# Performance work log

Measured on AMD Instinct MI355X. Metric: run time of the kernel, lower is better.

## Reference

```python
import jax, jax.numpy as jnp
import numpy as np

N, D, H, L, T, R = 50000, 128, 8, 2, 4, 8
E = 800000
HD = D // H  # head_size = 16
SQRT_D = float(np.sqrt(HD))


def typed_linear(x, types, W):
    # x: (n, Din), types: (n,), W: (T, Din, Dout)  -- per-type dense projection
    out = jnp.zeros((x.shape[0], W.shape[-1]), x.dtype)
    for t in range(W.shape[0]):
        out = out + jnp.where((types == t)[:, None], x @ W[t], 0.0)
    return out


def rel_typed(x, etype, W):
    # x: (E, H, d), etype: (E,), W: (H, R, d, d) -- per-head, per-edge-type linear
    out = jnp.zeros_like(x)
    for r in range(W.shape[1]):
        out = out + jnp.where((etype == r)[:, None, None], jnp.einsum('ehd,hdo->eho', x, W[:, r]), 0.0)
    return out


def edge_softmax(a, dst, n):
    # softmax over incoming edges per destination node, per head. a: (E, H)
    amax = jax.ops.segment_max(a, dst, num_segments=n)
    amax = jnp.where(jnp.isfinite(amax), amax, 0.0)
    ex = jnp.exp(a - amax[dst])
    s = jax.ops.segment_sum(ex, dst, num_segments=n)
    return ex / (s[dst] + 1e-9)


def layer_norm(x, g, b, eps=1e-5):
    mu = x.mean(-1, keepdims=True)
    var = ((x - mu) ** 2).mean(-1, keepdims=True)
    return (x - mu) * jax.lax.rsqrt(var + eps) * g + b


def hgt_conv(x, ntype, etype, src, dst, Wk, Wq, Wv, Wa, ratt, rmsg, rpri, skip):
    n = x.shape[0]
    k = typed_linear(x, ntype, Wk).reshape(n, H, HD)
    q = typed_linear(x, ntype, Wq).reshape(n, H, HD)
    v = typed_linear(x, ntype, Wv).reshape(n, H, HD)
    kw = rel_typed(k[src], etype, ratt)               # (E, H, d)
    pri = rpri[:, etype].T                            # (E, H)
    a = (kw * q[dst]).sum(-1) * pri / SQRT_D          # (E, H)
    m = rel_typed(v[src], etype, rmsg)                # (E, H, d)
    att = edge_softmax(a, dst, n)                     # (E, H)
    h = jax.ops.segment_sum(m * att[..., None], dst, num_segments=n)
    h = h.reshape(n, D)
    h = typed_linear(h, ntype, Wa)                    # dropout off (eval)
    alpha = jax.nn.sigmoid(skip[ntype])[:, None]
    return h * alpha + x * (1.0 - alpha)


def setup_inputs() -> dict:
    key = jax.random.key(0)
    ks = jax.random.split(key, 12)
    g_lin = float(np.sqrt(2.0 / (D + D)))   # xavier-ish scale for D x D
    g_rel = float(np.sqrt(2.0 / (HD + HD)))
    g_emb = float(np.sqrt(2.0 / (N + D)))
    return {
        'embed': jax.random.normal(ks[0], (T, N, D), jnp.float32) * g_emb,
        'Wk': jax.random.normal(ks[1], (L, T, D, D), jnp.float32) * g_lin,
        'Wq': jax.random.normal(ks[2], (L, T, D, D), jnp.float32) * g_lin,
        'Wv': jax.random.normal(ks[3], (L, T, D, D), jnp.float32) * g_lin,
        'Wa': jax.random.normal(ks[4], (L, T, D, D), jnp.float32) * g_lin,
        'rel_att': jax.random.normal(ks[5], (L, H, R, HD, HD), jnp.float32) * g_rel,
        'rel_msg': jax.random.normal(ks[6], (L, H, R, HD, HD), jnp.float32) * g_rel,
        'rel_pri': jnp.ones((L, H, R), jnp.float32),
        'skip': jnp.ones((L, T), jnp.float32),
        'ln_g': jnp.ones((L, D), jnp.float32),
        'ln_b': jnp.zeros((L, D), jnp.float32),
        'src': jax.random.randint(ks[7], (E,), 0, N, jnp.int32),
        'dst': jax.random.randint(ks[8], (E,), 0, N, jnp.int32),
        'ntype': jax.random.randint(ks[9], (N,), 0, T, jnp.int32),
        'etype': jax.random.randint(ks[10], (E,), 0, R, jnp.int32),
    }


def reference(embed, Wk, Wq, Wv, Wa, rel_att, rel_msg, rel_pri, skip, ln_g, ln_b, src, dst, ntype, etype):
    # masked per-type embedding init: node gets row <rank-within-its-type> of its type table
    onehot = jax.nn.one_hot(ntype, T, dtype=jnp.int32)
    rank = jnp.take_along_axis(jnp.cumsum(onehot, axis=0), ntype[:, None], axis=1)[:, 0] - 1
    h = embed[ntype, rank]                            # (N, D)
    for l in range(L):
        h_prev = h
        hc = hgt_conv(h, ntype, etype, src, dst,
                      Wk[l], Wq[l], Wv[l], Wa[l],
                      rel_att[l], rel_msg[l], rel_pri[l], skip[l])
        h = layer_norm(hc, ln_g[l], ln_b[l]) + h_prev
    return h
```

## Files before the change

### kernel.cpp

```cpp
#include <hip/hip_runtime.h>
#include <math.h>

#define N_NODES 50000
#define DIM     128
#define NHEAD   8
#define HDIM    16
#define NLAYER  2
#define NTYPE   4
#define NREL    8
#define NEDGE   800000
#define RB      256
#define MT      32
#define NK      (N_NODES * NREL)
#define LHR     (NLAYER * NHEAD * NREL)

typedef __attribute__((ext_vector_type(8))) short bf16x8;
typedef __attribute__((ext_vector_type(4))) float f32x4;

__device__ __forceinline__ float blo(unsigned w) { return __uint_as_float(w << 16); }
__device__ __forceinline__ float bhi(unsigned w) { return __uint_as_float(w & 0xFFFF0000u); }
__device__ __forceinline__ unsigned short f2bf(float f) {
    unsigned b = __float_as_uint(f);
    b += 0x7FFFu + ((b >> 16) & 1u);
    return (unsigned short)(b >> 16);
}
__device__ __forceinline__ bf16x8 pack8(float4 x0, float4 x1) {
    bf16x8 r;
    r[0] = (short)f2bf(x0.x); r[1] = (short)f2bf(x0.y);
    r[2] = (short)f2bf(x0.z); r[3] = (short)f2bf(x0.w);
    r[4] = (short)f2bf(x1.x); r[5] = (short)f2bf(x1.y);
    r[6] = (short)f2bf(x1.z); r[7] = (short)f2bf(x1.w);
    return r;
}
__device__ __forceinline__ bf16x8 zero8() {
    bf16x8 r;
    #pragma unroll
    for (int j = 0; j < 8; j++) r[j] = 0;
    return r;
}


__global__ void k_hist(const int* __restrict__ ntype, int* __restrict__ hist, int n) {
    __shared__ int cnt[NTYPE];
    if (threadIdx.x < NTYPE) cnt[threadIdx.x] = 0;
    __syncthreads();
    int i = blockIdx.x * RB + threadIdx.x;
    if (i < n) atomicAdd(&cnt[ntype[i]], 1);
    __syncthreads();
    if (threadIdx.x < NTYPE) hist[blockIdx.x * NTYPE + threadIdx.x] = cnt[threadIdx.x];
}

__global__ void k_prefix(const int* __restrict__ hist, int* __restrict__ off, int nb) {
    int t = threadIdx.x;
    if (t >= NTYPE) return;
    int acc = 0;
    for (int b = 0; b < nb; b++) { off[b * NTYPE + t] = acc; acc += hist[b * NTYPE + t]; }
}

__global__ void k_rank(const int* __restrict__ ntype, const int* __restrict__ off,
                       int* __restrict__ rank, int n) {
    __shared__ int ty[RB];
    int i = blockIdx.x * RB + threadIdx.x;
    int t = (i < n) ? ntype[i] : -1;
    ty[threadIdx.x] = t;
    __syncthreads();
    if (i < n) {
        int c = 0;
        for (int j = 0; j < (int)threadIdx.x; j++) c += (ty[j] == t);
        rank[i] = off[blockIdx.x * NTYPE + t] + c;
    }
}

__global__ void k_embed(const float* __restrict__ embed, const int* __restrict__ ntype,
                        const int* __restrict__ rank, float* __restrict__ h) {
    int i = blockIdx.x;
    int t = ntype[i], r = rank[i];
    h[(size_t)i * DIM + threadIdx.x] = embed[((size_t)t * N_NODES + r) * DIM + threadIdx.x];
}

__global__ void k_typeoff(const int* __restrict__ hist, const int* __restrict__ boff,
                          int nb, int* __restrict__ typeoff) {
    if (threadIdx.x == 0 && blockIdx.x == 0) {
        int acc = 0;
        for (int t = 0; t < NTYPE; t++) {
            typeoff[t] = acc;
            acc += boff[(nb - 1) * NTYPE + t] + hist[(nb - 1) * NTYPE + t];
        }
    }
}

__global__ void k_perm(const int* __restrict__ ntype, const int* __restrict__ rank,
                       const int* __restrict__ typeoff, int* __restrict__ perm,
                       int* __restrict__ iperm, int n) {
    int i = blockIdx.x * 256 + threadIdx.x;
    if (i < n) {
        int p = typeoff[ntype[i]] + rank[i];
        perm[p] = i;
        iperm[i] = p;
    }
}


__global__ void k_deg2(const int* __restrict__ dst, const int* __restrict__ etype,
                       int* __restrict__ deg) {
    int e = blockIdx.x * 256 + threadIdx.x;
    if (e < NEDGE) atomicAdd(&deg[dst[e] * NREL + etype[e]], 1);
}

__global__ void k_scan1(const int* __restrict__ deg, int* __restrict__ rs,
                        int* __restrict__ bsum, int n) {
    __shared__ int sh[256];
    int i = blockIdx.x * 256 + threadIdx.x;
    int v = (i < n) ? deg[i] : 0;
    sh[threadIdx.x] = v;
    __syncthreads();
    for (int off = 1; off < 256; off <<= 1) {
        int x = (threadIdx.x >= off) ? sh[threadIdx.x - off] : 0;
        __syncthreads();
        sh[threadIdx.x] += x;
        __syncthreads();
    }
    if (i < n) rs[i] = sh[threadIdx.x] - v;
    if (threadIdx.x == 255) bsum[blockIdx.x] = sh[255];
}

__global__ void k_scan2b(int* __restrict__ bsum, int nb) {
    __shared__ int sh[256];
    __shared__ int carry;
    if (threadIdx.x == 0) carry = 0;
    __syncthreads();
    for (int base = 0; base < nb; base += 256) {
        int i = base + threadIdx.x;
        int v = (i < nb) ? bsum[i] : 0;
        sh[threadIdx.x] = v;
        __syncthreads();
        for (int off = 1; off < 256; off <<= 1) {
            int x = (threadIdx.x >= off) ? sh[threadIdx.x - off] : 0;
            __syncthreads();
            sh[threadIdx.x] += x;
            __syncthreads();
        }
        if (i < nb) bsum[i] = sh[threadIdx.x] - v + carry;
        __syncthreads();
        if (threadIdx.x == 0) carry += sh[255];
        __syncthreads();
    }
}

__global__ void k_scan3(int* __restrict__ rs, const int* __restrict__ bsum, int n) {
    int i = blockIdx.x * 256 + threadIdx.x;
    if (i < n) rs[i] += bsum[blockIdx.x];
    if (i == 0) rs[n] = NEDGE;
}

__global__ void k_scatter2(const int* __restrict__ src, const int* __restrict__ dst,
                           const int* __restrict__ etype, const int* __restrict__ iperm,
                           const int* __restrict__ rs,
                           int* __restrict__ cur, int* __restrict__ epk) {
    int e = blockIdx.x * 256 + threadIdx.x;
    if (e < NEDGE) {
        int et = etype[e];
        int key = dst[e] * NREL + et;
        int p = atomicAdd(&cur[key], 1);
        epk[rs[key] + p] = iperm[src[e]] | (et << 24);
    }
}


__global__ void k_rattB(const float* __restrict__ ratt, unsigned short* __restrict__ rattB) {
    int i = blockIdx.x * 256 + threadIdx.x;
    rattB[i] = f2bf(ratt[i]);
}

__global__ void k_rmsgT(const float* __restrict__ rmsg, float* __restrict__ rmsgT) {
    int b = blockIdx.x;
    int d = threadIdx.x >> 4, o = threadIdx.x & 15;
    rmsgT[b * 256 + o * 16 + d] = rmsg[b * 256 + d * 16 + o];
}

__global__ void k_rmsgBP(const float* __restrict__ rmsg, unsigned short* __restrict__ out) {
    int b = blockIdx.x;
    int i = threadIdx.x;
    int ln = i >> 3, e = i & 7;
    int half = ln >> 4;
    unsigned short v = 0;
    if (half < 2) v = f2bf(rmsg[(size_t)b * 256 + (half * 8 + e) * 16 + (ln & 15)]);
    out[(size_t)b * 512 + i] = v;
}

__global__ void k_rattBP(const float* __restrict__ ratt, const float* __restrict__ rpri,
                         unsigned short* __restrict__ out) {
    int b = blockIdx.x;
    int i = threadIdx.x;
    int ln = i >> 3, e = i & 7;
    int half = ln >> 4;
    int et = b % NREL;
    int hh = (b / NREL) % NHEAD;
    int l = b / (NREL * NHEAD);
    float scale = rpri[(l * NHEAD + hh) * NREL + et] * 0.25f;
    unsigned short v = 0;
    if (half < 2) v = f2bf(ratt[(size_t)b * 256 + (half * 8 + e) * 16 + (ln & 15)] * scale);
    out[(size_t)b * 512 + i] = v;
}

__global__ void k_packW_all(const float* __restrict__ Wk, const float* __restrict__ Wq,
                            const float* __restrict__ Wv, const float* __restrict__ Wa,
                            unsigned short* __restrict__ wpk) {
    int bid = blockIdx.x;
    int t = bid & 3;
    int m = (bid >> 2) & 3;
    int l = bid >> 4;
    const float* W = (m == 0 ? Wk : (m == 1 ? Wq : (m == 2 ? Wv : Wa)))
                     + ((size_t)l * NTYPE + t) * 16384;
    unsigned short* ob = wpk + (size_t)bid * 16384;
    for (int idx = threadIdx.x; idx < 16384; idx += 256) {
        int ct = idx >> 11, kc = (idx >> 9) & 3, ln = (idx >> 3) & 63, j = idx & 7;
        int k = kc * 32 + ((ln >> 4) << 3) + j;
        int c = ct * 16 + (ln & 15);
        ob[idx] = f2bf(W[k * 128 + c]);
    }
}


template<int FULL>
__global__ __launch_bounds__(256) void k_qkv_mfma(
        const float* __restrict__ h, const int* __restrict__ perm, const int* __restrict__ ntype,
        const float* __restrict__ Wk, const float* __restrict__ Wq, const float* __restrict__ Wv,
        const unsigned short* __restrict__ WkB, const unsigned short* __restrict__ WqB,
        const unsigned short* __restrict__ WvB,
        const unsigned short* __restrict__ rattBP, const unsigned short* __restrict__ rmsgBP,
        const float* __restrict__ rmsgT,
        unsigned short* __restrict__ kb, float* __restrict__ qout,
        unsigned short* __restrict__ vt, unsigned short* __restrict__ tab, int n) {
    int tid = threadIdx.x;
    int base = blockIdx.x * MT;
    __shared__ int nodes_s[MT];
    __shared__ int types_s[MT];
    __shared__ unsigned short pool[MT][272];

    if (tid < MT) {
        int idx = base + tid;
        int nd = (idx < n) ? perm[idx] : -1;
        nodes_s[tid] = nd;
        types_s[tid] = (nd >= 0) ? ntype[nd] : -1;
    }
    __syncthreads();
    bool same = (nodes_s[MT - 1] >= 0) && (types_s[0] == types_s[MT - 1]);
    int l = tid & 63, w = tid >> 6;

    if (same) {
        int t = types_s[0];
        const unsigned short* wbk = WkB + (size_t)t * 16384;
        const unsigned short* wbq = WqB + (size_t)t * 16384;
        const unsigned short* wbv = WvB + (size_t)t * 16384;
        f32x4 acc[3][2][2];
        #pragma unroll
        for (int m = 0; m < 3; m++)
            #pragma unroll
            for (int a = 0; a < 2; a++)
                #pragma unroll
                for (int b = 0; b < 2; b++) {
                    acc[m][a][b][0] = 0.f; acc[m][a][b][1] = 0.f;
                    acc[m][a][b][2] = 0.f; acc[m][a][b][3] = 0.f;
                }
        #pragma unroll 1
        for (int kc = 0; kc < 4; kc++) {
            int koff = kc * 32 + ((l >> 4) << 3);
            int r0 = l & 15;
            const float4* p0 = (const float4*)(h + (size_t)nodes_s[r0] * DIM + koff);
            bf16x8 a0 = pack8(p0[0], p0[1]);
            const float4* p1 = (const float4*)(h + (size_t)nodes_s[16 + r0] * DIM + koff);
            bf16x8 a1 = pack8(p1[0], p1[1]);
            #pragma unroll
            for (int cti = 0; cti < 2; cti++) {
                int boff = ((w * 2 + cti) * 4 + kc) * 512 + l * 8;
                bf16x8 bk = *(const bf16x8*)(wbk + boff);
                acc[0][0][cti] = __builtin_amdgcn_mfma_f32_16x16x32_bf16(a0, bk, acc[0][0][cti], 0, 0, 0);
                acc[0][1][cti] = __builtin_amdgcn_mfma_f32_16x16x32_bf16(a1, bk, acc[0][1][cti], 0, 0, 0);
                bf16x8 bq = *(const bf16x8*)(wbq + boff);
                acc[1][0][cti] = __builtin_amdgcn_mfma_f32_16x16x32_bf16(a0, bq, acc[1][0][cti], 0, 0, 0);
                acc[1][1][cti] = __builtin_amdgcn_mfma_f32_16x16x32_bf16(a1, bq, acc[1][1][cti], 0, 0, 0);
                bf16x8 bv = *(const bf16x8*)(wbv + boff);
                acc[2][0][cti] = __builtin_amdgcn_mfma_f32_16x16x32_bf16(a0, bv, acc[2][0][cti], 0, 0, 0);
                acc[2][1][cti] = __builtin_amdgcn_mfma_f32_16x16x32_bf16(a1, bv, acc[2][1][cti], 0, 0, 0);
            }
        }
        #pragma unroll
        for (int mt = 0; mt < 2; mt++)
            #pragma unroll
            for (int cti = 0; cti < 2; cti++) {
                int col = w * 32 + cti * 16 + (l & 15);
                #pragma unroll
                for (int r = 0; r < 4; r++) {
                    int row = mt * 16 + ((l >> 4) << 2) + r;
                    size_t p = (size_t)(base + row) * DIM + col;
                    qout[p] = acc[1][mt][cti][r];
                    pool[row][136 + col] = f2bf(acc[2][mt][cti][r]);
                    unsigned short kv = f2bf(acc[0][mt][cti][r]);
                    pool[row][col] = kv;
                    if constexpr (!FULL) kb[p] = kv;
                }
            }
    } else {
        int o = tid & 127, half = tid >> 7;
        for (int nn = half; nn < MT; nn += 2) {
            int nd = nodes_s[nn];
            if (nd < 0) { pool[nn][136 + o] = 0; pool[nn][o] = 0; continue; }
            int t = types_s[nn];
            const float* wk = Wk + (size_t)t * 16384;
            const float* wq = Wq + (size_t)t * 16384;
            const float* wv = Wv + (size_t)t * 16384;
            float ak = 0.f, aq = 0.f, av = 0.f;
            for (int d = 0; d < DIM; d++) {
                float xv = h[(size_t)nd * DIM + d];
                ak = fmaf(xv, wk[d * DIM + o], ak);
                aq = fmaf(xv, wq[d * DIM + o], aq);
                av = fmaf(xv, wv[d * DIM + o], av);
            }
            size_t p = (size_t)(base + nn) * DIM + o;
            qout[p] = aq;
            pool[nn][136 + o] = f2bf(av);
            unsigned short kv = f2bf(ak);
            pool[nn][o] = kv;
            if constexpr (!FULL) kb[p] = kv;
        }
    }
    __syncthreads();

    if constexpr (FULL) {
        int half = l >> 4;
        bf16x8 afrk[2][2], afrv[2][2];
        #pragma unroll
        for (int hh2 = 0; hh2 < 2; hh2++) {
            int hh = w * 2 + hh2;
            #pragma unroll
            for (int nt = 0; nt < 2; nt++) {
                if (half < 2) {
                    afrk[hh2][nt] = *(const bf16x8*)&pool[nt * 16 + (l & 15)][hh * HDIM + half * 8];
                    afrv[hh2][nt] = *(const bf16x8*)&pool[nt * 16 + (l & 15)][136 + hh * HDIM + half * 8];
                } else {
                    afrk[hh2][nt] = zero8();
                    afrv[hh2][nt] = zero8();
                }
            }
        }
        __syncthreads();
        #pragma unroll 1
        for (int et = 0; et < NREL; et++) {
            #pragma unroll
            for (int hh2 = 0; hh2 < 2; hh2++) {
                int hh = w * 2 + hh2;
                bf16x8 bfa = *(const bf16x8*)(rattBP + ((size_t)(hh * NREL + et) * 64 + l) * 8);
                bf16x8 bfm = *(const bf16x8*)(rmsgBP + ((size_t)(hh * NREL + et) * 64 + l) * 8);
                #pragma unroll
                for (int nt = 0; nt < 2; nt++) {
                    f32x4 dk = {0.f, 0.f, 0.f, 0.f};
                    dk = __builtin_amdgcn_mfma_f32_16x16x32_bf16(afrk[hh2][nt], bfa, dk, 0, 0, 0);
                    f32x4 dv = {0.f, 0.f, 0.f, 0.f};
                    dv = __builtin_amdgcn_mfma_f32_16x16x32_bf16(afrv[hh2][nt], bfm, dv, 0, 0, 0);
                    #pragma unroll
                    for (int r = 0; r < 4; r++) {
                        int row = nt * 16 + half * 4 + r;
                        pool[row][hh * HDIM + (l & 15)] = f2bf(dk[r]);
                        pool[row][128 + hh * HDIM + (l & 15)] = f2bf(dv[r]);
                    }
                }
            }
            __syncthreads();
            #pragma unroll
            for (int it = 0; it < 4; it++) {
                int idx = it * 256 + tid;
                int row = idx >> 5;
                int c8 = idx & 31;
                if (base + row < n)
                    *(uint4*)&tab[((size_t)(base + row) * NREL + et) * 256 + c8 * 8] =
                        *(const uint4*)&pool[row][c8 * 8];
            }
            __syncthreads();
        }
    } else {
        int o = tid & 127, half = tid >> 7;
        int hh = o >> 4, oo = o & 15;
        #pragma unroll 1
        for (int et = 0; et < NREL; et++) {
            const float4* wm4 = (const float4*)(rmsgT + ((size_t)(hh * NREL + et) * HDIM + oo) * HDIM);
            float4 m0 = wm4[0], m1 = wm4[1], m2 = wm4[2], m3 = wm4[3];
            for (int i = 0; i < 16; i++) {
                int nn = half * 16 + i;
                if (base + nn >= n) continue;
                const uint4* vr = (const uint4*)&pool[nn][136 + hh * HDIM];
                uint4 v0 = vr[0], v1 = vr[1];
                float vv = blo(v0.x)*m0.x + bhi(v0.x)*m0.y + blo(v0.y)*m0.z + bhi(v0.y)*m0.w
                         + blo(v0.z)*m1.x + bhi(v0.z)*m1.y + blo(v0.w)*m1.z + bhi(v0.w)*m1.w
                         + blo(v1.x)*m2.x + bhi(v1.x)*m2.y + blo(v1.y)*m2.z + bhi(v1.y)*m2.w
                         + blo(v1.z)*m3.x + bhi(v1.z)*m3.y + blo(v1.w)*m3.z + bhi(v1.w)*m3.w;
                vt[((size_t)(base + nn) * NREL + et) * DIM + o] = f2bf(vv);
            }
        }
    }
}


__global__ __launch_bounds__(128) void k_fused12(
        const unsigned short* __restrict__ tab, const float* __restrict__ qbuf,
        const int* __restrict__ perm,
        const int* __restrict__ rs2, const int* __restrict__ epk,
        float* __restrict__ agg) {
    int b = blockIdx.x;
    int node = perm[b];
    int tid = threadIdx.x;
    int hh = tid >> 4, oo = tid & 15;
    int wv = tid >> 6;
    int hl = hh & 3;

    __shared__ float q_s[DIM];
    __shared__ float a_sw[2][4][HDIM + 1];
    __shared__ int   es_sw[2][HDIM];

    int e0 = rs2[node * NREL];
    int e1 = rs2[node * NREL + NREL];
    if (e0 == e1) { agg[(size_t)b * DIM + tid] = 0.f; return; }

    q_s[tid] = qbuf[(size_t)b * DIM + tid];
    const float4* q4 = (const float4*)&q_s[hh * HDIM];
    float4 q0 = q4[0], q1 = q4[1], q2 = q4[2], q3 = q4[3];

    float m_h = -1e30f, s_h = 0.f, out = 0.f;

    for (int w0e = e0; w0e < e1; w0e += HDIM) {
        int cnt = min(HDIM, e1 - w0e);
        float a = -1e30f;
        int pk = 0;
        if (oo < cnt) {
            pk = epk[w0e + oo];
            int sv = pk & 0x00FFFFFF;
            int et = ((unsigned)pk) >> 24;
            const uint4* kw = (const uint4*)(tab + ((size_t)sv * NREL + et) * 256 + hh * HDIM);
            uint4 ka = kw[0], kc = kw[1];
            a = blo(ka.x)*q0.x + bhi(ka.x)*q0.y + blo(ka.y)*q0.z + bhi(ka.y)*q0.w
              + blo(ka.z)*q1.x + bhi(ka.z)*q1.y + blo(ka.w)*q1.z + bhi(ka.w)*q1.w
              + blo(kc.x)*q2.x + bhi(kc.x)*q2.y + blo(kc.y)*q2.z + bhi(kc.y)*q2.w
              + blo(kc.z)*q3.x + bhi(kc.z)*q3.y + blo(kc.w)*q3.z + bhi(kc.w)*q3.w;
        }
        if (hl == 0) es_sw[wv][oo] = pk;
        float cmax = a;
        cmax = fmaxf(cmax, __shfl_xor(cmax, 1));
        cmax = fmaxf(cmax, __shfl_xor(cmax, 2));
        cmax = fmaxf(cmax, __shfl_xor(cmax, 4));
        cmax = fmaxf(cmax, __shfl_xor(cmax, 8));
        float m_t = (cmax > m_h + 12.f) ? cmax : m_h;
        float r = __expf(m_h - m_t);
        s_h *= r; out *= r; m_h = m_t;
        float p = (oo < cnt) ? __expf(a - m_h) : 0.f;
        float ps = p;
        ps += __shfl_xor(ps, 1);
        ps += __shfl_xor(ps, 2);
        ps += __shfl_xor(ps, 4);
        ps += __shfl_xor(ps, 8);
        s_h += ps;
        a_sw[wv][hl][oo] = p;
        for (int c = 0; c < cnt; c++) {
            float pc = a_sw[wv][hl][c];
            int pkc = es_sw[wv][c];
            int sv = pkc & 0x00FFFFFF;
            int et = ((unsigned)pkc) >> 24;
            unsigned short uv = tab[((size_t)sv * NREL + et) * 256 + 128 + tid];
            out = fmaf(pc, __uint_as_float((unsigned)uv << 16), out);
        }
    }

    agg[(size_t)b * DIM + tid] = out / (s_h + 1e-9f);
}


__global__ __launch_bounds__(128) void k_fused11(
        const unsigned short* __restrict__ kb, const float* __restrict__ qbuf,
        const unsigned short* __restrict__ vt,
        const int* __restrict__ perm,
        const int* __restrict__ rs2, const int* __restrict__ epk,
        const unsigned short* __restrict__ rattB, const float* __restrict__ rpri,
        float* __restrict__ agg) {
    int b = blockIdx.x;
    int node = perm[b];
    int tid = threadIdx.x;
    int hh = tid >> 4, oo = tid & 15;
    int wv = tid >> 6;
    int hl = hh & 3;

    __shared__ float q_s[DIM];
    __shared__ float u_s[NREL][NHEAD * HDIM + 4];
    __shared__ float a_sw[2][4][HDIM + 1];
    __shared__ int   es_sw[2][HDIM];

    int e0 = rs2[node * NREL];
    int e1 = rs2[node * NREL + NREL];
    if (e0 == e1) { agg[(size_t)b * DIM + tid] = 0.f; return; }

    q_s[tid] = qbuf[(size_t)b * DIM + tid];
    {
        const float4* q4 = (const float4*)&q_s[hh * HDIM];
        float4 q0 = q4[0], q1 = q4[1], q2 = q4[2], q3 = q4[3];
        #pragma unroll
        for (int et = 0; et < NREL; et++) {
            const uint4* wB = (const uint4*)(rattB + ((size_t)(hh * NREL + et) * HDIM + oo) * HDIM);
            uint4 wa = wB[0], wb = wB[1];
            float s = blo(wa.x)*q0.x + bhi(wa.x)*q0.y + blo(wa.y)*q0.z + bhi(wa.y)*q0.w
                    + blo(wa.z)*q1.x + bhi(wa.z)*q1.y + blo(wa.w)*q1.z + bhi(wa.w)*q1.w
                    + blo(wb.x)*q2.x + bhi(wb.x)*q2.y + blo(wb.y)*q2.z + bhi(wb.y)*q2.w
                    + blo(wb.z)*q3.x + bhi(wb.z)*q3.y + blo(wb.w)*q3.z + bhi(wb.w)*q3.w;
            u_s[et][tid] = s * rpri[hh * NREL + et] * 0.25f;
        }
    }

    float m_h = -1e30f, s_h = 0.f, out = 0.f;

    for (int w0e = e0; w0e < e1; w0e += HDIM) {
        int cnt = min(HDIM, e1 - w0e);
        float a = -1e30f;
        int pk = 0;
        if (oo < cnt) {
            pk = epk[w0e + oo];
            int sv = pk & 0x00FFFFFF;
            int et = ((unsigned)pk) >> 24;
            const uint4* kr = (const uint4*)(kb + (size_t)sv * DIM + hh * HDIM);
            uint4 ka = kr[0], kc = kr[1];
            const float4* u4 = (const float4*)&u_s[et][hh * HDIM];
            float4 u0 = u4[0], u1 = u4[1], u2 = u4[2], u3 = u4[3];
            a = blo(ka.x)*u0.x + bhi(ka.x)*u0.y + blo(ka.y)*u0.z + bhi(ka.y)*u0.w
              + blo(ka.z)*u1.x + bhi(ka.z)*u1.y + blo(ka.w)*u1.z + bhi(ka.w)*u1.w
              + blo(kc.x)*u2.x + bhi(kc.x)*u2.y + blo(kc.y)*u2.z + bhi(kc.y)*u2.w
              + blo(kc.z)*u3.x + bhi(kc.z)*u3.y + blo(kc.w)*u3.z + bhi(kc.w)*u3.w;
        }
        if (hl == 0) es_sw[wv][oo] = pk;
        float cmax = a;
        cmax = fmaxf(cmax, __shfl_xor(cmax, 1));
        cmax = fmaxf(cmax, __shfl_xor(cmax, 2));
        cmax = fmaxf(cmax, __shfl_xor(cmax, 4));
        cmax = fmaxf(cmax, __shfl_xor(cmax, 8));
        float m_t = (cmax > m_h + 12.f) ? cmax : m_h;
        float r = __expf(m_h - m_t);
        s_h *= r; out *= r; m_h = m_t;
        float p = (oo < cnt) ? __expf(a - m_h) : 0.f;
        float ps = p;
        ps += __shfl_xor(ps, 1);
        ps += __shfl_xor(ps, 2);
        ps += __shfl_xor(ps, 4);
        ps += __shfl_xor(ps, 8);
        s_h += ps;
        a_sw[wv][hl][oo] = p;
        for (int c = 0; c < cnt; c++) {
            float pc = a_sw[wv][hl][c];
            int pkc = es_sw[wv][c];
            int sv = pkc & 0x00FFFFFF;
            int et = ((unsigned)pkc) >> 24;
            unsigned short uv = vt[((size_t)sv * NREL + et) * DIM + tid];
            out = fmaf(pc, __uint_as_float((unsigned)uv << 16), out);
        }
    }

    agg[(size_t)b * DIM + tid] = out / (s_h + 1e-9f);
}


__global__ __launch_bounds__(256) void k_out_mfma(
        const float* __restrict__ agg, float* __restrict__ h,
        const int* __restrict__ perm, const int* __restrict__ ntype,
        const float* __restrict__ Wa, const unsigned short* __restrict__ WaB,
        const float* __restrict__ skip,
        const float* __restrict__ ln_g, const float* __restrict__ ln_b, int n) {
    int tid = threadIdx.x;
    int base = blockIdx.x * MT;
    __shared__ int nodes_s[MT];
    __shared__ int types_s[MT];
    __shared__ float hc[MT][132];
    __shared__ float mu_s[MT], rsg[MT];

    if (tid < MT) {
        int idx = base + tid;
        int nd = (idx < n) ? perm[idx] : -1;
        nodes_s[tid] = nd;
        types_s[tid] = (nd >= 0) ? ntype[nd] : -1;
    }
    __syncthreads();
    bool same = (nodes_s[MT - 1] >= 0) && (types_s[0] == types_s[MT - 1]);
    int l = tid & 63, w = tid >> 6;

    if (same) {
        int t = types_s[0];
        const unsigned short* wb = WaB + (size_t)t * 16384;
        f32x4 acc[2][2];
        #pragma unroll
        for (int a = 0; a < 2; a++)
            #pragma unroll
            for (int b = 0; b < 2; b++) {
                acc[a][b][0] = 0.f; acc[a][b][1] = 0.f;
                acc[a][b][2] = 0.f; acc[a][b][3] = 0.f;
            }
        #pragma unroll 1
        for (int kc = 0; kc < 4; kc++) {
            int koff = kc * 32 + ((l >> 4) << 3);
            int r0 = l & 15;
            const float4* p0 = (const float4*)(agg + (size_t)(base + r0) * DIM + koff);
            bf16x8 a0 = pack8(p0[0], p0[1]);
            const float4* p1 = (const float4*)(agg + (size_t)(base + 16 + r0) * DIM + koff);
            bf16x8 a1 = pack8(p1[0], p1[1]);
            #pragma unroll
            for (int cti = 0; cti < 2; cti++) {
                int boff = ((w * 2 + cti) * 4 + kc) * 512 + l * 8;
                bf16x8 bw = *(const bf16x8*)(wb + boff);
                acc[0][cti] = __builtin_amdgcn_mfma_f32_16x16x32_bf16(a0, bw, acc[0][cti], 0, 0, 0);
                acc[1][cti] = __builtin_amdgcn_mfma_f32_16x16x32_bf16(a1, bw, acc[1][cti], 0, 0, 0);
            }
        }
        float alpha = 1.f / (1.f + __expf(-skip[t]));
        #pragma unroll
        for (int mt = 0; mt < 2; mt++)
            #pragma unroll
            for (int cti = 0; cti < 2; cti++) {
                int col = w * 32 + cti * 16 + (l & 15);
                #pragma unroll
                for (int r = 0; r < 4; r++) {
                    int row = mt * 16 + ((l >> 4) << 2) + r;
                    float hp = h[(size_t)nodes_s[row] * DIM + col];
                    hc[row][col] = acc[mt][cti][r] * alpha + hp * (1.f - alpha);
                }
            }
    } else {
        int o = tid & 127, half = tid >> 7;
        for (int nn = half; nn < MT; nn += 2) {
            int nd = nodes_s[nn];
            if (nd < 0) continue;
            int t = types_s[nn];
            const float* wv = Wa + (size_t)t * 16384;
            float a0 = 0.f;
            for (int d = 0; d < DIM; d++)
                a0 = fmaf(agg[(size_t)(base + nn) * DIM + d], wv[d * DIM + o], a0);
            float alpha = 1.f / (1.f + __expf(-skip[t]));
            float hp = h[(size_t)nd * DIM + o];
            hc[nn][o] = a0 * alpha + hp * (1.f - alpha);
        }
    }
    __syncthreads();
    {
        int row = tid >> 3, j = tid & 7;
        if (nodes_s[row] >= 0) {
            float s = 0.f;
            for (int d = j; d < DIM; d += 8) s += hc[row][d];
            s += __shfl_xor(s, 1);
            s += __shfl_xor(s, 2);
            s += __shfl_xor(s, 4);
            float mu = s * (1.f / DIM);
            float v = 0.f;
            for (int d = j; d < DIM; d += 8) { float dv = hc[row][d] - mu; v = fmaf(dv, dv, v); }
            v += __shfl_xor(v, 1);
            v += __shfl_xor(v, 2);
            v += __shfl_xor(v, 4);
            if (j == 0) { mu_s[row] = mu; rsg[row] = rsqrtf(v * (1.f / DIM) + 1e-5f); }
        }
    }
    __syncthreads();
    {
        int row = tid >> 3, j = tid & 7;
        int nd = nodes_s[row];
        if (nd >= 0) {
            float mu = mu_s[row], rs = rsg[row];
            #pragma unroll
            for (int c = 0; c < 16; c++) {
                int col = j * 16 + c;
                float hp = h[(size_t)nd * DIM + col];
                h[(size_t)nd * DIM + col] = (hc[row][col] - mu) * rs * ln_g[col] + ln_b[col] + hp;
            }
        }
    }
}


extern "C" void kernel_launch(void* const* d_in, const int* in_sizes, int n_in,
                              void* d_out, int out_size, void* d_ws, size_t ws_size,
                              hipStream_t stream) {
    const float* embed = (const float*)d_in[0];
    const float* Wk    = (const float*)d_in[1];
    const float* Wq    = (const float*)d_in[2];
    const float* Wv    = (const float*)d_in[3];
    const float* Wa    = (const float*)d_in[4];
    const float* ratt  = (const float*)d_in[5];
    const float* rmsg  = (const float*)d_in[6];
    const float* rpri  = (const float*)d_in[7];
    const float* skip  = (const float*)d_in[8];
    const float* ln_g  = (const float*)d_in[9];
    const float* ln_b  = (const float*)d_in[10];
    const int*   src   = (const int*)d_in[11];
    const int*   dst   = (const int*)d_in[12];
    const int*   ntype = (const int*)d_in[13];
    const int*   etype = (const int*)d_in[14];

    float* h = (float*)d_out;

    const size_t ND = (size_t)N_NODES * DIM;
    const int nb = (N_NODES + RB - 1) / RB;
    unsigned short* kb = (unsigned short*)d_ws;
    float* qbuf = (float*)(kb + ND);
    int* rs2  = (int*)(qbuf + ND);
    int* deg2 = rs2 + (NK + 1);
    int* cur2 = deg2 + NK;
    int* epk  = cur2 + NK;
    int* bsum = epk + NEDGE;
    int* rank = bsum + 2048;
    int* hist = rank + N_NODES;
    int* boff = hist + nb * NTYPE;
    int* typeoff = boff + nb * NTYPE;
    int* perm = typeoff + NTYPE;
    int* iperm = perm + N_NODES;
    float* rmsgT = (float*)(iperm + N_NODES);
    unsigned short* rattB  = (unsigned short*)(rmsgT + (size_t)LHR * 256);
    unsigned short* rattBP = rattB + (size_t)LHR * 256;
    unsigned short* rmsgBP = rattBP + (size_t)LHR * 512;
    unsigned short* wpk = rmsgBP + (size_t)LHR * 512;
    unsigned short* vt  = wpk + (size_t)NLAYER * 4 * NTYPE * 16384;
    unsigned short* tab = vt;
    size_t need_full = (size_t)((char*)(tab + (size_t)N_NODES * NREL * 256) - (char*)d_ws);
    const bool FULL = (ws_size >= need_full);
    float* agg = qbuf;

    const int EB = (NEDGE + 255) / 256;
    const int nb2 = (NK + 255) / 256;

    k_hist<<<nb, RB, 0, stream>>>(ntype, hist, N_NODES);
    k_prefix<<<1, 64, 0, stream>>>(hist, boff, nb);
    k_rank<<<nb, RB, 0, stream>>>(ntype, boff, rank, N_NODES);
    k_embed<<<N_NODES, DIM, 0, stream>>>(embed, ntype, rank, h);
    k_typeoff<<<1, 64, 0, stream>>>(hist, boff, nb, typeoff);
    k_perm<<<nb, 256, 0, stream>>>(ntype, rank, typeoff, perm, iperm, N_NODES);

    hipMemsetAsync(deg2, 0, (size_t)NK * sizeof(int), stream);
    hipMemsetAsync(cur2, 0, (size_t)NK * sizeof(int), stream);
    k_deg2<<<EB, 256, 0, stream>>>(dst, etype, deg2);
    k_scan1<<<nb2, 256, 0, stream>>>(deg2, rs2, bsum, NK);
    k_scan2b<<<1, 256, 0, stream>>>(bsum, nb2);
    k_scan3<<<nb2, 256, 0, stream>>>(rs2, bsum, NK);
    k_scatter2<<<EB, 256, 0, stream>>>(src, dst, etype, iperm, rs2, cur2, epk);

    k_rmsgT<<<LHR, 256, 0, stream>>>(rmsg, rmsgT);
    k_rattB<<<LHR, 256, 0, stream>>>(ratt, rattB);
    k_rattBP<<<LHR, 512, 0, stream>>>(ratt, rpri, rattBP);
    k_rmsgBP<<<LHR, 512, 0, stream>>>(rmsg, rmsgBP);
    k_packW_all<<<NLAYER * 4 * NTYPE, 256, 0, stream>>>(Wk, Wq, Wv, Wa, wpk);

    const int NMB = (N_NODES + MT - 1) / MT;

    for (int l = 0; l < NLAYER; l++) {
        const float* Wk_l = Wk + (size_t)l * NTYPE * DIM * DIM;
        const float* Wq_l = Wq + (size_t)l * NTYPE * DIM * DIM;
        const float* Wv_l = Wv + (size_t)l * NTYPE * DIM * DIM;
        const float* Wa_l = Wa + (size_t)l * NTYPE * DIM * DIM;
        const unsigned short* wkB_l = wpk + ((size_t)l * 4 + 0) * NTYPE * 16384;
        const unsigned short* wqB_l = wpk + ((size_t)l * 4 + 1) * NTYPE * 16384;
        const unsigned short* wvB_l = wpk + ((size_t)l * 4 + 2) * NTYPE * 16384;
        const unsigned short* waB_l = wpk + ((size_t)l * 4 + 3) * NTYPE * 16384;
        const unsigned short* rattB_l  = rattB + (size_t)l * NHEAD * NREL * 256;
        const unsigned short* rattBP_l = rattBP + (size_t)l * NHEAD * NREL * 512;
        const unsigned short* rmsgBP_l = rmsgBP + (size_t)l * NHEAD * NREL * 512;
        const float* rmsgT_l = rmsgT + (size_t)l * NHEAD * NREL * 256;
        const float* rpri_l = rpri + (size_t)l * NHEAD * NREL;
        const float* skip_l = skip + (size_t)l * NTYPE;
        const float* g_l = ln_g + (size_t)l * DIM;
        const float* b_l = ln_b + (size_t)l * DIM;

        if (FULL) {
            k_qkv_mfma<1><<<NMB, 256, 0, stream>>>(h, perm, ntype, Wk_l, Wq_l, Wv_l,
                                                   wkB_l, wqB_l, wvB_l,
                                                   rattBP_l, rmsgBP_l, rmsgT_l,
                                                   kb, qbuf, vt, tab, N_NODES);
            k_fused12<<<N_NODES, 128, 0, stream>>>(tab, qbuf, perm, rs2, epk, agg);
        } else {
            k_qkv_mfma<0><<<NMB, 256, 0, stream>>>(h, perm, ntype, Wk_l, Wq_l, Wv_l,
                                                   wkB_l, wqB_l, wvB_l,
                                                   rattBP_l, rmsgBP_l, rmsgT_l,
                                                   kb, qbuf, vt, tab, N_NODES);
            k_fused11<<<N_NODES, 128, 0, stream>>>(kb, qbuf, vt, perm, rs2, epk,
                                                   rattB_l, rpri_l, agg);
        }
        k_out_mfma<<<NMB, 256, 0, stream>>>(agg, h, perm, ntype, Wa_l, waB_l,
                                            skip_l, g_l, b_l, N_NODES);
    }
}
```

Baseline: 726.7 us.

## Keep node features in type-sorted order across layers, unpermute at end

Hidden state is now stored in a workspace buffer ordered by the type-sorted permutation, so the QKV and output projection kernels read and write contiguous rows instead of gathering through perm. The embedding is gathered straight into permuted order, and a final kernel scatters rows back to the original order. The shared pool in the QKV kernel is split into separate K, V and table arrays, which drops one barrier. This adds an extra workspace buffer and a final copy pass.

```diff
diff --git a/kernel.cpp b/kernel.cpp
--- a/kernel.cpp
+++ b/kernel.cpp
@@ -71,13 +71,6 @@
     }
 }
 
-__global__ void k_embed(const float* __restrict__ embed, const int* __restrict__ ntype,
-                        const int* __restrict__ rank, float* __restrict__ h) {
-    int i = blockIdx.x;
-    int t = ntype[i], r = rank[i];
-    h[(size_t)i * DIM + threadIdx.x] = embed[((size_t)t * N_NODES + r) * DIM + threadIdx.x];
-}
-
 __global__ void k_typeoff(const int* __restrict__ hist, const int* __restrict__ boff,
                           int nb, int* __restrict__ typeoff) {
     if (threadIdx.x == 0 && blockIdx.x == 0) {
@@ -98,6 +91,21 @@
         perm[p] = i;
         iperm[i] = p;
     }
+}
+
+__global__ void k_embed2(const float* __restrict__ embed, const int* __restrict__ perm,
+                         const int* __restrict__ ntype, const int* __restrict__ rank,
+                         float* __restrict__ hbuf) {
+    int p = blockIdx.x;
+    int node = perm[p];
+    int t = ntype[node], r = rank[node];
+    hbuf[(size_t)p * DIM + threadIdx.x] = embed[((size_t)t * N_NODES + r) * DIM + threadIdx.x];
+}
+
+__global__ void k_final(const float* __restrict__ hbuf, const int* __restrict__ perm,
+                        float* __restrict__ out) {
+    int p = blockIdx.x;
+    out[(size_t)perm[p] * DIM + threadIdx.x] = hbuf[(size_t)p * DIM + threadIdx.x];
 }
 
 
@@ -234,18 +242,19 @@
         unsigned short* __restrict__ vt, unsigned short* __restrict__ tab, int n) {
     int tid = threadIdx.x;
     int base = blockIdx.x * MT;
-    __shared__ int nodes_s[MT];
     __shared__ int types_s[MT];
-    __shared__ unsigned short pool[MT][272];
+    __shared__ int valid_s[MT];
+    __shared__ unsigned short vs[MT][136];
+    __shared__ unsigned short ks[MT][136];
 
     if (tid < MT) {
         int idx = base + tid;
         int nd = (idx < n) ? perm[idx] : -1;
-        nodes_s[tid] = nd;
+        valid_s[tid] = nd;
         types_s[tid] = (nd >= 0) ? ntype[nd] : -1;
     }
     __syncthreads();
-    bool same = (nodes_s[MT - 1] >= 0) && (types_s[0] == types_s[MT - 1]);
+    bool same = (valid_s[MT - 1] >= 0) && (types_s[0] == types_s[MT - 1]);
     int l = tid & 63, w = tid >> 6;
 
     if (same) {
@@ -267,9 +276,9 @@
         for (int kc = 0; kc < 4; kc++) {
             int koff = kc * 32 + ((l >> 4) << 3);
             int r0 = l & 15;
-            const float4* p0 = (const float4*)(h + (size_t)nodes_s[r0] * DIM + koff);
+            const float4* p0 = (const float4*)(h + (size_t)(base + r0) * DIM + koff);
             bf16x8 a0 = pack8(p0[0], p0[1]);
-            const float4* p1 = (const float4*)(h + (size_t)nodes_s[16 + r0] * DIM + koff);
+            const float4* p1 = (const float4*)(h + (size_t)(base + 16 + r0) * DIM + koff);
             bf16x8 a1 = pack8(p1[0], p1[1]);
             #pragma unroll
             for (int cti = 0; cti < 2; cti++) {
@@ -295,39 +304,39 @@
                     int row = mt * 16 + ((l >> 4) << 2) + r;
                     size_t p = (size_t)(base + row) * DIM + col;
                     qout[p] = acc[1][mt][cti][r];
-                    pool[row][136 + col] = f2bf(acc[2][mt][cti][r]);
+                    vs[row][col] = f2bf(acc[2][mt][cti][r]);
                     unsigned short kv = f2bf(acc[0][mt][cti][r]);
-                    pool[row][col] = kv;
+                    ks[row][col] = kv;
                     if constexpr (!FULL) kb[p] = kv;
                 }
             }
     } else {
         int o = tid & 127, half = tid >> 7;
         for (int nn = half; nn < MT; nn += 2) {
-            int nd = nodes_s[nn];
-            if (nd < 0) { pool[nn][136 + o] = 0; pool[nn][o] = 0; continue; }
+            if (valid_s[nn] < 0) { vs[nn][o] = 0; ks[nn][o] = 0; continue; }
             int t = types_s[nn];
             const float* wk = Wk + (size_t)t * 16384;
             const float* wq = Wq + (size_t)t * 16384;
             const float* wv = Wv + (size_t)t * 16384;
             float ak = 0.f, aq = 0.f, av = 0.f;
             for (int d = 0; d < DIM; d++) {
-                float xv = h[(size_t)nd * DIM + d];
+                float xv = h[(size_t)(base + nn) * DIM + d];
                 ak = fmaf(xv, wk[d * DIM + o], ak);
                 aq = fmaf(xv, wq[d * DIM + o], aq);
                 av = fmaf(xv, wv[d * DIM + o], av);
             }
             size_t p = (size_t)(base + nn) * DIM + o;
             qout[p] = aq;
-            pool[nn][136 + o] = f2bf(av);
+            vs[nn][o] = f2bf(av);
             unsigned short kv = f2bf(ak);
-            pool[nn][o] = kv;
+            ks[nn][o] = kv;
             if constexpr (!FULL) kb[p] = kv;
         }
     }
     __syncthreads();
 
     if constexpr (FULL) {
+        __shared__ unsigned short tab_s[MT][264];
         int half = l >> 4;
         bf16x8 afrk[2][2], afrv[2][2];
         #pragma unroll
@@ -336,15 +345,14 @@
             #pragma unroll
             for (int nt = 0; nt < 2; nt++) {
                 if (half < 2) {
-                    afrk[hh2][nt] = *(const bf16x8*)&pool[nt * 16 + (l & 15)][hh * HDIM + half * 8];
-                    afrv[hh2][nt] = *(const bf16x8*)&pool[nt * 16 + (l & 15)][136 + hh * HDIM + half * 8];
+                    afrk[hh2][nt] = *(const bf16x8*)&ks[nt * 16 + (l & 15)][hh * HDIM + half * 8];
+                    afrv[hh2][nt] = *(const bf16x8*)&vs[nt * 16 + (l & 15)][hh * HDIM + half * 8];
                 } else {
                     afrk[hh2][nt] = zero8();
                     afrv[hh2][nt] = zero8();
                 }
             }
         }
-        __syncthreads();
         #pragma unroll 1
         for (int et = 0; et < NREL; et++) {
             #pragma unroll
@@ -361,8 +369,8 @@
                     #pragma unroll
                     for (int r = 0; r < 4; r++) {
                         int row = nt * 16 + half * 4 + r;
-                        pool[row][hh * HDIM + (l & 15)] = f2bf(dk[r]);
-                        pool[row][128 + hh * HDIM + (l & 15)] = f2bf(dv[r]);
+                        tab_s[row][hh * HDIM + (l & 15)] = f2bf(dk[r]);
+                        tab_s[row][128 + hh * HDIM + (l & 15)] = f2bf(dv[r]);
                     }
                 }
             }
@@ -374,7 +382,7 @@
                 int c8 = idx & 31;
                 if (base + row < n)
                     *(uint4*)&tab[((size_t)(base + row) * NREL + et) * 256 + c8 * 8] =
-                        *(const uint4*)&pool[row][c8 * 8];
+                        *(const uint4*)&tab_s[row][c8 * 8];
             }
             __syncthreads();
         }
@@ -388,7 +396,7 @@
             for (int i = 0; i < 16; i++) {
                 int nn = half * 16 + i;
                 if (base + nn >= n) continue;
-                const uint4* vr = (const uint4*)&pool[nn][136 + hh * HDIM];
+                const uint4* vr = (const uint4*)&vs[nn][hh * HDIM];
                 uint4 v0 = vr[0], v1 = vr[1];
                 float vv = blo(v0.x)*m0.x + bhi(v0.x)*m0.y + blo(v0.y)*m0.z + bhi(v0.y)*m0.w
                          + blo(v0.z)*m1.x + bhi(v0.z)*m1.y + blo(v0.w)*m1.z + bhi(v0.w)*m1.w
@@ -570,19 +578,19 @@
         const float* __restrict__ ln_g, const float* __restrict__ ln_b, int n) {
     int tid = threadIdx.x;
     int base = blockIdx.x * MT;
-    __shared__ int nodes_s[MT];
     __shared__ int types_s[MT];
+    __shared__ int valid_s[MT];
     __shared__ float hc[MT][132];
     __shared__ float mu_s[MT], rsg[MT];
 
     if (tid < MT) {
         int idx = base + tid;
         int nd = (idx < n) ? perm[idx] : -1;
-        nodes_s[tid] = nd;
+        valid_s[tid] = nd;
         types_s[tid] = (nd >= 0) ? ntype[nd] : -1;
     }
     __syncthreads();
-    bool same = (nodes_s[MT - 1] >= 0) && (types_s[0] == types_s[MT - 1]);
+    bool same = (valid_s[MT - 1] >= 0) && (types_s[0] == types_s[MT - 1]);
     int l = tid & 63, w = tid >> 6;
 
     if (same) {
@@ -621,29 +629,28 @@
                 #pragma unroll
                 for (int r = 0; r < 4; r++) {
                     int row = mt * 16 + ((l >> 4) << 2) + r;
-                    float hp = h[(size_t)nodes_s[row] * DIM + col];
+                    float hp = h[(size_t)(base + row) * DIM + col];
                     hc[row][col] = acc[mt][cti][r] * alpha + hp * (1.f - alpha);
                 }
             }
     } else {
         int o = tid & 127, half = tid >> 7;
         for (int nn = half; nn < MT; nn += 2) {
-            int nd = nodes_s[nn];
-            if (nd < 0) continue;
+            if (valid_s[nn] < 0) continue;
             int t = types_s[nn];
             const float* wv = Wa + (size_t)t * 16384;
             float a0 = 0.f;
             for (int d = 0; d < DIM; d++)
                 a0 = fmaf(agg[(size_t)(base + nn) * DIM + d], wv[d * DIM + o], a0);
             float alpha = 1.f / (1.f + __expf(-skip[t]));
-            float hp = h[(size_t)nd * DIM + o];
+            float hp = h[(size_t)(base + nn) * DIM + o];
             hc[nn][o] = a0 * alpha + hp * (1.f - alpha);
         }
     }
     __syncthreads();
     {
         int row = tid >> 3, j = tid & 7;
-        if (nodes_s[row] >= 0) {
+        if (valid_s[row] >= 0) {
             float s = 0.f;
             for (int d = j; d < DIM; d += 8) s += hc[row][d];
             s += __shfl_xor(s, 1);
@@ -661,14 +668,14 @@
     __syncthreads();
     {
         int row = tid >> 3, j = tid & 7;
-        int nd = nodes_s[row];
-        if (nd >= 0) {
+        if (valid_s[row] >= 0) {
             float mu = mu_s[row], rs = rsg[row];
             #pragma unroll
             for (int c = 0; c < 16; c++) {
                 int col = j * 16 + c;
-                float hp = h[(size_t)nd * DIM + col];
-                h[(size_t)nd * DIM + col] = (hc[row][col] - mu) * rs * ln_g[col] + ln_b[col] + hp;
+                size_t p = (size_t)(base + row) * DIM + col;
+                float hp = h[p];
+                h[p] = (hc[row][col] - mu) * rs * ln_g[col] + ln_b[col] + hp;
             }
         }
     }
@@ -694,13 +701,14 @@
     const int*   ntype = (const int*)d_in[13];
     const int*   etype = (const int*)d_in[14];
 
-    float* h = (float*)d_out;
+    float* out = (float*)d_out;
 
     const size_t ND = (size_t)N_NODES * DIM;
     const int nb = (N_NODES + RB - 1) / RB;
     unsigned short* kb = (unsigned short*)d_ws;
     float* qbuf = (float*)(kb + ND);
-    int* rs2  = (int*)(qbuf + ND);
+    float* hbuf = qbuf + ND;
+    int* rs2  = (int*)(hbuf + ND);
     int* deg2 = rs2 + (NK + 1);
     int* cur2 = deg2 + NK;
     int* epk  = cur2 + NK;
@@ -728,9 +736,9 @@
     k_hist<<<nb, RB, 0, stream>>>(ntype, hist, N_NODES);
     k_prefix<<<1, 64, 0, stream>>>(hist, boff, nb);
     k_rank<<<nb, RB, 0, stream>>>(ntype, boff, rank, N_NODES);
-    k_embed<<<N_NODES, DIM, 0, stream>>>(embed, ntype, rank, h);
     k_typeoff<<<1, 64, 0, stream>>>(hist, boff, nb, typeoff);
     k_perm<<<nb, 256, 0, stream>>>(ntype, rank, typeoff, perm, iperm, N_NODES);
+    k_embed2<<<N_NODES, DIM, 0, stream>>>(embed, perm, ntype, rank, hbuf);
 
     hipMemsetAsync(deg2, 0, (size_t)NK * sizeof(int), stream);
     hipMemsetAsync(cur2, 0, (size_t)NK * sizeof(int), stream);
@@ -767,20 +775,22 @@
         const float* b_l = ln_b + (size_t)l * DIM;
 
         if (FULL) {
-            k_qkv_mfma<1><<<NMB, 256, 0, stream>>>(h, perm, ntype, Wk_l, Wq_l, Wv_l,
+            k_qkv_mfma<1><<<NMB, 256, 0, stream>>>(hbuf, perm, ntype, Wk_l, Wq_l, Wv_l,
                                                    wkB_l, wqB_l, wvB_l,
                                                    rattBP_l, rmsgBP_l, rmsgT_l,
                                                    kb, qbuf, vt, tab, N_NODES);
             k_fused12<<<N_NODES, 128, 0, stream>>>(tab, qbuf, perm, rs2, epk, agg);
         } else {
-            k_qkv_mfma<0><<<NMB, 256, 0, stream>>>(h, perm, ntype, Wk_l, Wq_l, Wv_l,
+            k_qkv_mfma<0><<<NMB, 256, 0, stream>>>(hbuf, perm, ntype, Wk_l, Wq_l, Wv_l,
                                                    wkB_l, wqB_l, wvB_l,
                                                    rattBP_l, rmsgBP_l, rmsgT_l,
                                                    kb, qbuf, vt, tab, N_NODES);
             k_fused11<<<N_NODES, 128, 0, stream>>>(kb, qbuf, vt, perm, rs2, epk,
                                                    rattB_l, rpri_l, agg);
         }
-        k_out_mfma<<<NMB, 256, 0, stream>>>(agg, h, perm, ntype, Wa_l, waB_l,
+        k_out_mfma<<<NMB, 256, 0, stream>>>(agg, hbuf, perm, ntype, Wa_l, waB_l,
                                             skip_l, g_l, b_l, N_NODES);
     }
-}
+
+    k_final<<<N_NODES, DIM, 0, stream>>>(hbuf, perm, out);
+}
```

Result: slower. 768.9 us (+5.8%).
